# Optimization experiments

Hardware: AMD Instinct MI355X
Metric: run time of the kernel (lower is better)

The kernel has to match this reference:

```python
import jax, jax.numpy as jnp
import numpy as np

GAMMA = 0.8
RESCALE_ROT = 1.0
WEIGHT_PC = 0.5


def quat2mat(q):
    """q: [..., 4] (w,x,y,z) -> homogeneous rotation matrix [..., 4, 4]."""
    q = q / jnp.linalg.norm(q, axis=-1, keepdims=True)
    w, x, y, z = q[..., 0], q[..., 1], q[..., 2], q[..., 3]
    R3 = jnp.stack([
        jnp.stack([1 - 2 * y * y - 2 * z * z, 2 * x * y - 2 * z * w, 2 * x * z + 2 * y * w], -1),
        jnp.stack([2 * x * y + 2 * z * w, 1 - 2 * x * x - 2 * z * z, 2 * y * z - 2 * x * w], -1),
        jnp.stack([2 * x * z - 2 * y * w, 2 * y * z + 2 * x * w, 1 - 2 * x * x - 2 * y * y], -1),
    ], -2)  # [..., 3, 3]
    M = jnp.zeros(q.shape[:-1] + (4, 4), q.dtype)
    M = M.at[..., :3, :3].set(R3)
    M = M.at[..., 3, 3].set(1.0)
    return M


def tvector2mat(t):
    """t: [..., 3] -> homogeneous translation matrix [..., 4, 4]."""
    M = jnp.broadcast_to(jnp.eye(4, dtype=t.dtype), t.shape[:-1] + (4, 4))
    return M.at[..., :3, 3].set(t)


def quat_distance(q, r):
    """Geodesic distance 2*atan2(||vec(q*r^-1)||, |w(q*r^-1)|); q, r: [..., 4]."""
    rinv = r * jnp.array([1.0, -1.0, -1.0, -1.0], r.dtype)
    q0, q1, q2, q3 = q[..., 0], q[..., 1], q[..., 2], q[..., 3]
    r0, r1, r2, r3 = rinv[..., 0], rinv[..., 1], rinv[..., 2], rinv[..., 3]
    t0 = r0 * q0 - r1 * q1 - r2 * q2 - r3 * q3
    t1 = r0 * q1 + r1 * q0 - r2 * q3 + r3 * q2
    t2 = r0 * q2 + r1 * q3 + r2 * q0 - r3 * q1
    t3 = r0 * q3 - r1 * q2 + r2 * q1 + r3 * q0
    return 2.0 * jnp.arctan2(jnp.sqrt(t1 * t1 + t2 * t2 + t3 * t3), jnp.abs(t0))


def setup_inputs() -> dict:
    key = jax.random.key(0)
    kpc, kt, kr, kp = jax.random.split(key, 4)
    B, N, P = 16, 262144, 6
    xyz = jax.random.normal(kpc, (B, 3, N), dtype=jnp.float32) * 20.0
    point_clouds = jnp.concatenate([xyz, jnp.ones((B, 1, N), jnp.float32)], axis=1)  # [B,4,N] homogeneous
    target_transl = jax.random.normal(kt, (B, 3), dtype=jnp.float32)
    target_rot = jax.random.normal(kr, (B, 4), dtype=jnp.float32)
    target_rot = target_rot / jnp.linalg.norm(target_rot, axis=-1, keepdims=True)
    rot_list = jax.random.normal(kp, (P, B, 4), dtype=jnp.float32)
    rot_list = rot_list / jnp.linalg.norm(rot_list, axis=-1, keepdims=True)
    return {"point_clouds": point_clouds, "target_transl": target_transl,
            "target_rot": target_rot, "rot_list": rot_list}


def reference(point_clouds, target_transl, target_rot, rot_list):
    B = point_clouds.shape[0]
    P = rot_list.shape[0]

    T = tvector2mat(target_transl)                  # [B,4,4]
    RT_target = T @ quat2mat(target_rot)            # [B,4,4]
    RT_pred = jnp.einsum('bij,pbjk->pbik', T, quat2mat(rot_list))  # [P,B,4,4]

    # RT_total = RT_target^-1 @ RT_pred; rotate_forward applies RT_total^-1 to PC
    M = jnp.einsum('bij,pbjk->pbik', jnp.linalg.inv(RT_target), RT_pred)
    Minv = jnp.linalg.inv(M)                        # [P,B,4,4]
    pc_out = jnp.einsum('pbij,bjn->pbin', Minv, point_clouds)       # [P,B,4,N]
    err = jnp.linalg.norm(pc_out - point_clouds[None], axis=2)      # [P,B,N]
    pcl_per_pred = err.mean(axis=-1).sum(axis=-1)   # [P] sum over point clouds

    rot_per_pred = quat_distance(rot_list, target_rot[None]).mean(axis=-1)  # [P]

    # i_weight = gamma ** (P - 1 - i)
    w = jnp.power(jnp.float32(GAMMA), jnp.arange(P - 1, -1, -1, dtype=jnp.float32))
    pose = RESCALE_ROT * rot_per_pred
    total_i = (1.0 - WEIGHT_PC) * pose + WEIGHT_PC * (pcl_per_pred / B)

    total_loss = jnp.sum(w * total_i)
    rot_loss = jnp.sum(w * rot_per_pred)
    pcl_loss = jnp.sum(w * (pcl_per_pred / B))
    return jnp.stack([total_loss, rot_loss, pcl_loss])
```

## Files before the change

### kernel.cpp

```cpp
#include <hip/hip_runtime.h>
#include <math.h>

#define GAMMA 0.8f
#define RESCALE_ROT 1.0f
#define WEIGHT_PC 0.5f

__device__ inline void quat_to_R(float w, float x, float y, float z, float R[3][3]) {
    R[0][0] = 1.0f - 2.0f*y*y - 2.0f*z*z;
    R[0][1] = 2.0f*x*y - 2.0f*z*w;
    R[0][2] = 2.0f*x*z + 2.0f*y*w;
    R[1][0] = 2.0f*x*y + 2.0f*z*w;
    R[1][1] = 1.0f - 2.0f*x*x - 2.0f*z*z;
    R[1][2] = 2.0f*y*z - 2.0f*x*w;
    R[2][0] = 2.0f*x*z - 2.0f*y*w;
    R[2][1] = 2.0f*y*z + 2.0f*x*w;
    R[2][2] = 1.0f - 2.0f*x*x - 2.0f*y*y;
}

__global__ void setup_kernel(const float* __restrict__ target_rot,
                             const float* __restrict__ rot_list,
                             float* __restrict__ ws,
                             int B, int P, int N) {
    __shared__ float red[128];
    const int tid = threadIdx.x;
    float contrib = 0.0f;

    if (tid < P * B) {
        const int p = tid / B;
        const int b = tid - p * B;

        float w = 1.0f;
        for (int i = 0; i < P - 1 - p; ++i) w *= GAMMA;

        const float* qp = rot_list + (size_t)(p * B + b) * 4;
        const float* qt = target_rot + (size_t)b * 4;
        float pw = qp[0], px = qp[1], py = qp[2], pz = qp[3];
        float tw = qt[0], tx = qt[1], ty = qt[2], tz = qt[3];

        {
            float r0 = tw, r1 = -tx, r2 = -ty, r3 = -tz;
            float q0 = pw, q1 = px, q2 = py, q3 = pz;
            float t0 = r0*q0 - r1*q1 - r2*q2 - r3*q3;
            float t1 = r0*q1 + r1*q0 - r2*q3 + r3*q2;
            float t2 = r0*q2 + r1*q3 + r2*q0 - r3*q1;
            float t3 = r0*q3 - r1*q2 + r2*q1 + r3*q0;
            float d = 2.0f * atan2f(sqrtf(t1*t1 + t2*t2 + t3*t3), fabsf(t0));
            contrib = w * d / (float)B;
        }

        float ni = rsqrtf(pw*pw + px*px + py*py + pz*pz);
        pw *= ni; px *= ni; py *= ni; pz *= ni;
        ni = rsqrtf(tw*tw + tx*tx + ty*ty + tz*tz);
        tw *= ni; tx *= ni; ty *= ni; tz *= ni;

        float Rp[3][3], Rt[3][3], Rr[3][3];
        quat_to_R(pw, px, py, pz, Rp);
        quat_to_R(tw, tx, ty, tz, Rt);
        for (int i = 0; i < 3; ++i)
            for (int j = 0; j < 3; ++j)
                Rr[i][j] = Rp[0][i]*Rt[0][j] + Rp[1][i]*Rt[1][j] + Rp[2][i]*Rt[2][j];

        const float c  = w / ((float)B * (float)N);
        const float c2 = c * c;
        float* Q = ws + (size_t)(b * P + p) * 6;
        Q[0] = c2 * (2.0f - 2.0f * Rr[0][0]);
        Q[1] = c2 * (2.0f - 2.0f * Rr[1][1]);
        Q[2] = c2 * (2.0f - 2.0f * Rr[2][2]);
        Q[3] = c2 * (-2.0f * (Rr[0][1] + Rr[1][0]));
        Q[4] = c2 * (-2.0f * (Rr[0][2] + Rr[2][0]));
        Q[5] = c2 * (-2.0f * (Rr[1][2] + Rr[2][1]));
    }

    red[tid] = contrib;
    __syncthreads();
    if (tid == 0) {
        float s = 0.0f;
        for (int i = 0; i < P * B; ++i) s += red[i];
        ws[(size_t)B * P * 6 + 0] = 0.0f;
        ws[(size_t)B * P * 6 + 1] = s;
    }
}

template<int ITER, int PP>
__global__ __launch_bounds__(256) void pcl_kernel(const float* __restrict__ pc,
                                                  const float* __restrict__ wsQ,
                                                  float* __restrict__ acc,
                                                  int B, int N, int blocks_per_b) {
    __shared__ float Qs[PP * 6];
    const int tid = threadIdx.x;
    const int b     = blockIdx.x / blocks_per_b;
    const int chunk = blockIdx.x % blocks_per_b;

    if (tid < PP * 6) Qs[tid] = wsQ[(size_t)b * PP * 6 + tid];
    __syncthreads();

    float q[PP][6];
#pragma unroll
    for (int p = 0; p < PP; ++p)
#pragma unroll
        for (int j = 0; j < 6; ++j) q[p][j] = Qs[p * 6 + j];

    const int N4 = N >> 2;
    const float4* rx = (const float4*)(pc + (size_t)b * 4 * N);
    const float4* ry = rx + N4;
    const float4* rz = ry + N4;

    float sum = 0.0f;
#pragma unroll
    for (int k = 0; k < ITER; ++k) {
        int n4 = chunk * (ITER * 256) + k * 256 + tid;
        if (n4 < N4) {
            float4 vx = rx[n4];
            float4 vy = ry[n4];
            float4 vz = rz[n4];
            const float* fx = &vx.x;
            const float* fy = &vy.x;
            const float* fz = &vz.x;
#pragma unroll
            for (int e = 0; e < 4; ++e) {
                float x = fx[e], y = fy[e], z = fz[e];
                float xx = x*x, yy = y*y, zz = z*z;
                float xy = x*y, xz = x*z, yz = y*z;
#pragma unroll
                for (int p = 0; p < PP; ++p) {
                    float v = q[p][0]*xx + q[p][1]*yy + q[p][2]*zz
                            + q[p][3]*xy + q[p][4]*xz + q[p][5]*yz;
                    sum += sqrtf(fmaxf(v, 0.0f));
                }
            }
        }
    }

#pragma unroll
    for (int off = 32; off > 0; off >>= 1) sum += __shfl_down(sum, off, 64);
    __shared__ float wsum[4];
    if ((tid & 63) == 0) wsum[tid >> 6] = sum;
    __syncthreads();
    if (tid == 0) atomicAdd(acc, wsum[0] + wsum[1] + wsum[2] + wsum[3]);
}

__global__ __launch_bounds__(256) void pcl_kernel_gen(const float* __restrict__ pc,
                                                      const float* __restrict__ wsQ,
                                                      float* __restrict__ acc,
                                                      int B, int P, int N, int blocks_per_b) {
    extern __shared__ float Qs[];
    const int tid = threadIdx.x;
    const int b     = blockIdx.x / blocks_per_b;
    const int chunk = blockIdx.x % blocks_per_b;
    for (int i = tid; i < P * 6; i += 256) Qs[i] = wsQ[(size_t)b * P * 6 + i];
    __syncthreads();

    const int N4 = N >> 2;
    const float4* rx = (const float4*)(pc + (size_t)b * 4 * N);
    const float4* ry = rx + N4;
    const float4* rz = ry + N4;

    float sum = 0.0f;
    for (int k = 0; k < 4; ++k) {
        int n4 = chunk * (4 * 256) + k * 256 + tid;
        if (n4 < N4) {
            float4 vx = rx[n4]; float4 vy = ry[n4]; float4 vz = rz[n4];
            const float* fx = &vx.x; const float* fy = &vy.x; const float* fz = &vz.x;
            for (int e = 0; e < 4; ++e) {
                float x = fx[e], y = fy[e], z = fz[e];
                float xx = x*x, yy = y*y, zz = z*z;
                float xy = x*y, xz = x*z, yz = y*z;
                for (int p = 0; p < P; ++p) {
                    const float* qp = Qs + p * 6;
                    float v = qp[0]*xx + qp[1]*yy + qp[2]*zz
                            + qp[3]*xy + qp[4]*xz + qp[5]*yz;
                    sum += sqrtf(fmaxf(v, 0.0f));
                }
            }
        }
    }
#pragma unroll
    for (int off = 32; off > 0; off >>= 1) sum += __shfl_down(sum, off, 64);
    __shared__ float wsum[4];
    if ((tid & 63) == 0) wsum[tid >> 6] = sum;
    __syncthreads();
    if (tid == 0) atomicAdd(acc, wsum[0] + wsum[1] + wsum[2] + wsum[3]);
}

__global__ void finalize_kernel(const float* __restrict__ accs,
                                float* __restrict__ out) {
    float S_pcl = accs[0];
    float S_rot = accs[1];
    out[0] = (1.0f - WEIGHT_PC) * RESCALE_ROT * S_rot + WEIGHT_PC * S_pcl;
    out[1] = S_rot;
    out[2] = S_pcl;
}

extern "C" void kernel_launch(void* const* d_in, const int* in_sizes, int n_in,
                              void* d_out, int out_size, void* d_ws, size_t ws_size,
                              hipStream_t stream) {
    const float* pc = (const float*)d_in[0];
    const float* tr = (const float*)d_in[2];
    const float* rl = (const float*)d_in[3];
    float* out = (float*)d_out;
    float* ws  = (float*)d_ws;

    const int B = in_sizes[1] / 3;
    const int N = in_sizes[0] / (B * 4);
    const int P = in_sizes[3] / (B * 4);

    setup_kernel<<<1, 128, 0, stream>>>(tr, rl, ws, B, P, N);

    float* acc = ws + (size_t)B * P * 6;
    const int N4 = N >> 2;
    const int ITER = 4;
    const int per_block = ITER * 256;
    const int blocks_per_b = (N4 + per_block - 1) / per_block;

    if (P == 6) {
        pcl_kernel<ITER, 6><<<B * blocks_per_b, 256, 0, stream>>>(pc, ws, acc, B, N, blocks_per_b);
    } else {
        pcl_kernel_gen<<<B * blocks_per_b, 256, P * 6 * sizeof(float), stream>>>(pc, ws, acc, B, P, N, blocks_per_b);
    }

    finalize_kernel<<<1, 1, 0, stream>>>(acc, out);
}
```

Measured before the change: 110.2 us.

## Fuse setup into sweep kernel and replace atomics with per-block partials

Removes the separate setup kernel: each sweep block recomputes its per-batch quadratic-form coefficients from the quaternions in its first threads. The global atomicAdd per block is replaced by per-block partial writes, and a 256-thread finalize kernel reduces them and also computes the rotation loss. An EXACT template path drops the bounds check when N divides evenly. This saves one launch and the atomic contention, at the cost of redundant per-block setup math and a slightly larger final reduction.

```diff
diff --git a/kernel.cpp b/kernel.cpp
--- a/kernel.cpp
+++ b/kernel.cpp
@@ -17,81 +17,52 @@
     R[2][2] = 1.0f - 2.0f*x*x - 2.0f*y*y;
 }
 
-__global__ void setup_kernel(const float* __restrict__ target_rot,
-                             const float* __restrict__ rot_list,
-                             float* __restrict__ ws,
-                             int B, int P, int N) {
-    __shared__ float red[128];
-    const int tid = threadIdx.x;
-    float contrib = 0.0f;
-
-    if (tid < P * B) {
-        const int p = tid / B;
-        const int b = tid - p * B;
-
-        float w = 1.0f;
-        for (int i = 0; i < P - 1 - p; ++i) w *= GAMMA;
-
-        const float* qp = rot_list + (size_t)(p * B + b) * 4;
-        const float* qt = target_rot + (size_t)b * 4;
-        float pw = qp[0], px = qp[1], py = qp[2], pz = qp[3];
-        float tw = qt[0], tx = qt[1], ty = qt[2], tz = qt[3];
-
-        {
-            float r0 = tw, r1 = -tx, r2 = -ty, r3 = -tz;
-            float q0 = pw, q1 = px, q2 = py, q3 = pz;
-            float t0 = r0*q0 - r1*q1 - r2*q2 - r3*q3;
-            float t1 = r0*q1 + r1*q0 - r2*q3 + r3*q2;
-            float t2 = r0*q2 + r1*q3 + r2*q0 - r3*q1;
-            float t3 = r0*q3 - r1*q2 + r2*q1 + r3*q0;
-            float d = 2.0f * atan2f(sqrtf(t1*t1 + t2*t2 + t3*t3), fabsf(t0));
-            contrib = w * d / (float)B;
-        }
-
-        float ni = rsqrtf(pw*pw + px*px + py*py + pz*pz);
-        pw *= ni; px *= ni; py *= ni; pz *= ni;
-        ni = rsqrtf(tw*tw + tx*tx + ty*ty + tz*tz);
-        tw *= ni; tx *= ni; ty *= ni; tz *= ni;
-
-        float Rp[3][3], Rt[3][3], Rr[3][3];
-        quat_to_R(pw, px, py, pz, Rp);
-        quat_to_R(tw, tx, ty, tz, Rt);
-        for (int i = 0; i < 3; ++i)
-            for (int j = 0; j < 3; ++j)
-                Rr[i][j] = Rp[0][i]*Rt[0][j] + Rp[1][i]*Rt[1][j] + Rp[2][i]*Rt[2][j];
-
-        const float c  = w / ((float)B * (float)N);
-        const float c2 = c * c;
-        float* Q = ws + (size_t)(b * P + p) * 6;
-        Q[0] = c2 * (2.0f - 2.0f * Rr[0][0]);
-        Q[1] = c2 * (2.0f - 2.0f * Rr[1][1]);
-        Q[2] = c2 * (2.0f - 2.0f * Rr[2][2]);
-        Q[3] = c2 * (-2.0f * (Rr[0][1] + Rr[1][0]));
-        Q[4] = c2 * (-2.0f * (Rr[0][2] + Rr[2][0]));
-        Q[5] = c2 * (-2.0f * (Rr[1][2] + Rr[2][1]));
-    }
-
-    red[tid] = contrib;
-    __syncthreads();
-    if (tid == 0) {
-        float s = 0.0f;
-        for (int i = 0; i < P * B; ++i) s += red[i];
-        ws[(size_t)B * P * 6 + 0] = 0.0f;
-        ws[(size_t)B * P * 6 + 1] = s;
-    }
-}
-
-template<int ITER, int PP>
-__global__ __launch_bounds__(256) void pcl_kernel(const float* __restrict__ pc,
-                                                  const float* __restrict__ wsQ,
-                                                  float* __restrict__ acc,
-                                                  int B, int N, int blocks_per_b) {
+__device__ inline void compute_Q(const float* __restrict__ target_rot,
+                                 const float* __restrict__ rot_list,
+                                 int p, int b, int B, int P, int N,
+                                 float* __restrict__ Qout ) {
+    const float* qp = rot_list + (size_t)(p * B + b) * 4;
+    const float* qt = target_rot + (size_t)b * 4;
+    float pw = qp[0], px = qp[1], py = qp[2], pz = qp[3];
+    float tw = qt[0], tx = qt[1], ty = qt[2], tz = qt[3];
+
+    float w = 1.0f;
+    for (int i = 0; i < P - 1 - p; ++i) w *= GAMMA;
+
+    float ni = rsqrtf(pw*pw + px*px + py*py + pz*pz);
+    pw *= ni; px *= ni; py *= ni; pz *= ni;
+    ni = rsqrtf(tw*tw + tx*tx + ty*ty + tz*tz);
+    tw *= ni; tx *= ni; ty *= ni; tz *= ni;
+
+    float Rp[3][3], Rt[3][3], Rr[3][3];
+    quat_to_R(pw, px, py, pz, Rp);
+    quat_to_R(tw, tx, ty, tz, Rt);
+    for (int i = 0; i < 3; ++i)
+        for (int j = 0; j < 3; ++j)
+            Rr[i][j] = Rp[0][i]*Rt[0][j] + Rp[1][i]*Rt[1][j] + Rp[2][i]*Rt[2][j];
+
+    const float c  = w / ((float)B * (float)N);
+    const float c2 = c * c;
+    Qout[0] = c2 * (2.0f - 2.0f * Rr[0][0]);
+    Qout[1] = c2 * (2.0f - 2.0f * Rr[1][1]);
+    Qout[2] = c2 * (2.0f - 2.0f * Rr[2][2]);
+    Qout[3] = c2 * (-2.0f * (Rr[0][1] + Rr[1][0]));
+    Qout[4] = c2 * (-2.0f * (Rr[0][2] + Rr[2][0]));
+    Qout[5] = c2 * (-2.0f * (Rr[1][2] + Rr[2][1]));
+}
+
+template<int ITER, int PP, bool EXACT>
+__global__ __launch_bounds__(256) void sweep_kernel(const float* __restrict__ pc,
+                                                    const float* __restrict__ target_rot,
+                                                    const float* __restrict__ rot_list,
+                                                    float* __restrict__ partials,
+                                                    int B, int N, int blocks_per_b) {
     __shared__ float Qs[PP * 6];
-    const int tid = threadIdx.x;
+    const int tid   = threadIdx.x;
     const int b     = blockIdx.x / blocks_per_b;
     const int chunk = blockIdx.x % blocks_per_b;
 
-    if (tid < PP * 6) Qs[tid] = wsQ[(size_t)b * PP * 6 + tid];
+    if (tid < PP) compute_Q(target_rot, rot_list, tid, b, B, PP, N, Qs + tid * 6);
     __syncthreads();
 
     float q[PP][6];
@@ -109,7 +80,7 @@
 #pragma unroll
     for (int k = 0; k < ITER; ++k) {
         int n4 = chunk * (ITER * 256) + k * 256 + tid;
-        if (n4 < N4) {
+        if (EXACT || n4 < N4) {
             float4 vx = rx[n4];
             float4 vy = ry[n4];
             float4 vz = rz[n4];
@@ -136,18 +107,20 @@
     __shared__ float wsum[4];
     if ((tid & 63) == 0) wsum[tid >> 6] = sum;
     __syncthreads();
-    if (tid == 0) atomicAdd(acc, wsum[0] + wsum[1] + wsum[2] + wsum[3]);
-}
-
-__global__ __launch_bounds__(256) void pcl_kernel_gen(const float* __restrict__ pc,
-                                                      const float* __restrict__ wsQ,
-                                                      float* __restrict__ acc,
-                                                      int B, int P, int N, int blocks_per_b) {
+    if (tid == 0) partials[blockIdx.x] = wsum[0] + wsum[1] + wsum[2] + wsum[3];
+}
+
+__global__ __launch_bounds__(256) void sweep_kernel_gen(const float* __restrict__ pc,
+                                                        const float* __restrict__ target_rot,
+                                                        const float* __restrict__ rot_list,
+                                                        float* __restrict__ partials,
+                                                        int B, int P, int N, int blocks_per_b) {
     extern __shared__ float Qs[];
-    const int tid = threadIdx.x;
+    const int tid   = threadIdx.x;
     const int b     = blockIdx.x / blocks_per_b;
     const int chunk = blockIdx.x % blocks_per_b;
-    for (int i = tid; i < P * 6; i += 256) Qs[i] = wsQ[(size_t)b * P * 6 + i];
+
+    for (int p = tid; p < P; p += 256) compute_Q(target_rot, rot_list, p, b, B, P, N, Qs + p * 6);
     __syncthreads();
 
     const int N4 = N >> 2;
@@ -179,16 +152,53 @@
     __shared__ float wsum[4];
     if ((tid & 63) == 0) wsum[tid >> 6] = sum;
     __syncthreads();
-    if (tid == 0) atomicAdd(acc, wsum[0] + wsum[1] + wsum[2] + wsum[3]);
-}
-
-__global__ void finalize_kernel(const float* __restrict__ accs,
-                                float* __restrict__ out) {
-    float S_pcl = accs[0];
-    float S_rot = accs[1];
-    out[0] = (1.0f - WEIGHT_PC) * RESCALE_ROT * S_rot + WEIGHT_PC * S_pcl;
-    out[1] = S_rot;
-    out[2] = S_pcl;
+    if (tid == 0) partials[blockIdx.x] = wsum[0] + wsum[1] + wsum[2] + wsum[3];
+}
+
+__global__ __launch_bounds__(256) void finalize_kernel(const float* __restrict__ partials,
+                                                       int nparts,
+                                                       const float* __restrict__ target_rot,
+                                                       const float* __restrict__ rot_list,
+                                                       float* __restrict__ out,
+                                                       int B, int P) {
+    const int tid = threadIdx.x;
+
+    float s_pcl = 0.0f;
+    for (int i = tid; i < nparts; i += 256) s_pcl += partials[i];
+
+    float s_rot = 0.0f;
+    if (tid < P * B) {
+        const int p = tid / B;
+        const int b = tid - p * B;
+        float w = 1.0f;
+        for (int i = 0; i < P - 1 - p; ++i) w *= GAMMA;
+        const float* qp = rot_list + (size_t)(p * B + b) * 4;
+        const float* qt = target_rot + (size_t)b * 4;
+        float r0 = qt[0], r1 = -qt[1], r2 = -qt[2], r3 = -qt[3];
+        float q0 = qp[0], q1 = qp[1], q2 = qp[2], q3 = qp[3];
+        float t0 = r0*q0 - r1*q1 - r2*q2 - r3*q3;
+        float t1 = r0*q1 + r1*q0 - r2*q3 + r3*q2;
+        float t2 = r0*q2 + r1*q3 + r2*q0 - r3*q1;
+        float t3 = r0*q3 - r1*q2 + r2*q1 + r3*q0;
+        float d = 2.0f * atan2f(sqrtf(t1*t1 + t2*t2 + t3*t3), fabsf(t0));
+        s_rot = w * d / (float)B;
+    }
+
+#pragma unroll
+    for (int off = 32; off > 0; off >>= 1) {
+        s_pcl += __shfl_down(s_pcl, off, 64);
+        s_rot += __shfl_down(s_rot, off, 64);
+    }
+    __shared__ float wp[4], wr[4];
+    if ((tid & 63) == 0) { wp[tid >> 6] = s_pcl; wr[tid >> 6] = s_rot; }
+    __syncthreads();
+    if (tid == 0) {
+        float S_pcl = wp[0] + wp[1] + wp[2] + wp[3];
+        float S_rot = wr[0] + wr[1] + wr[2] + wr[3];
+        out[0] = (1.0f - WEIGHT_PC) * RESCALE_ROT * S_rot + WEIGHT_PC * S_pcl;
+        out[1] = S_rot;
+        out[2] = S_pcl;
+    }
 }
 
 extern "C" void kernel_launch(void* const* d_in, const int* in_sizes, int n_in,
@@ -204,19 +214,22 @@
     const int N = in_sizes[0] / (B * 4);
     const int P = in_sizes[3] / (B * 4);
 
-    setup_kernel<<<1, 128, 0, stream>>>(tr, rl, ws, B, P, N);
-
-    float* acc = ws + (size_t)B * P * 6;
     const int N4 = N >> 2;
     const int ITER = 4;
     const int per_block = ITER * 256;
     const int blocks_per_b = (N4 + per_block - 1) / per_block;
+    const int grid = B * blocks_per_b;
+
+    float* partials = ws;
 
     if (P == 6) {
-        pcl_kernel<ITER, 6><<<B * blocks_per_b, 256, 0, stream>>>(pc, ws, acc, B, N, blocks_per_b);
+        if (N4 % per_block == 0)
+            sweep_kernel<ITER, 6, true><<<grid, 256, 0, stream>>>(pc, tr, rl, partials, B, N, blocks_per_b);
+        else
+            sweep_kernel<ITER, 6, false><<<grid, 256, 0, stream>>>(pc, tr, rl, partials, B, N, blocks_per_b);
     } else {
-        pcl_kernel_gen<<<B * blocks_per_b, 256, P * 6 * sizeof(float), stream>>>(pc, ws, acc, B, P, N, blocks_per_b);
-    }
-
-    finalize_kernel<<<1, 1, 0, stream>>>(acc, out);
-}
+        sweep_kernel_gen<<<grid, 256, P * 6 * sizeof(float), stream>>>(pc, tr, rl, partials, B, P, N, blocks_per_b);
+    }
+
+    finalize_kernel<<<1, 256, 0, stream>>>(partials, grid, tr, rl, out, B, P);
+}
```

New measurement: 104.9 us. 4.8% less time.
